# Kernel optimization log

Hardware: AMD Instinct MI355X
Metric: run time of the kernel (lower is better)

## Reference

```python
import jax, jax.numpy as jnp
import numpy as np

N = 8192
IN_F = 128
OUT_F = 128
ALPHA = 0.2  # LeakyReLU negative slope
NEG_INF = -9e15


def setup_inputs() -> dict:
    key = jax.random.key(0)
    k1, k2, k3, k4 = jax.random.split(key, 4)
    h = jax.random.normal(k1, (N, IN_F), dtype=jnp.float32)
    adj = jax.random.randint(k2, (N, N), 0, 2, dtype=jnp.int32)
    # nn.Linear(in, out, bias=False).weight is (out, in); store as (in, out) for h @ W
    W = jax.random.normal(k3, (IN_F, OUT_F), dtype=jnp.float32) * (1.0 / np.sqrt(IN_F))
    # a: (2*out_features, 1), xavier_uniform with gain=1.414
    limit = 1.414 * np.sqrt(6.0 / (2 * OUT_F + 1))
    a = jax.random.uniform(k4, (2 * OUT_F, 1), dtype=jnp.float32, minval=-limit, maxval=limit)
    return {"h": h, "adj": adj, "W": W, "a": a}


def reference(h, adj, W, a):
    Wh = h @ W  # (N, OUT_F)
    a1 = a[:OUT_F, 0]   # score contribution from source node i
    a2 = a[OUT_F:, 0]   # score contribution from target node j
    # e_ij = leakyrelu(Wh_i . a1 + Wh_j . a2) -- avoids the O(N^2 * 2F) concat
    s1 = Wh @ a1  # (N,)
    s2 = Wh @ a2  # (N,)
    e = jax.nn.leaky_relu(s1[:, None] + s2[None, :], negative_slope=ALPHA)  # (N, N)
    masked = jnp.where(adj > 0, e, NEG_INF)
    attention = jax.nn.softmax(masked, axis=1)  # (N, N)
    # dropout is a no-op in eval mode
    h_prime = attention @ Wh  # (N, OUT_F)
    return jax.nn.elu(h_prime)  # concat=True -> ELU
```

## Files before the change

### kernel.cpp

```cpp
#include <hip/hip_runtime.h>
#include <cstdint>
#include <cstddef>


#define NROW 8192
#define FDIM 128

typedef _Float16 f16;
typedef f16 f16x8 __attribute__((ext_vector_type(8)));
typedef float f32x4 __attribute__((ext_vector_type(4)));
typedef float f32x16 __attribute__((ext_vector_type(16)));

#define WS_BP  (2u*1024u*1024u)
#define WS_S12 (4u*1024u*1024u)
#define WS_RC  (WS_S12 + 64u*1024u)
#define WS_EF  (WS_RC + 128u*1024u)
#define WS_M2  (WS_EF + 64u*1024u)
#define WS_PWS (WS_M2 + 4u*1024u)

__global__ __launch_bounds__(256) void kA_wh_pack(const float* __restrict__ h,
                                                  const float* __restrict__ W,
                                                  const float* __restrict__ a,
                                                  const int* __restrict__ adj,
                                                  f16* __restrict__ Bp,
                                                  unsigned* __restrict__ bm,
                                                  float2* __restrict__ s12,
                                                  float* __restrict__ M2v) {
  __shared__ float smem[4736];
  const int bid = (int)blockIdx.x;
  const int t = (int)threadIdx.x;

  if (bid >= 256) {
    const int pb = bid - 256;
    const int w = t >> 6, l = t & 63;
    const int r = pb * 4 + w;
    const int rg = r >> 5, m = r & 31;
    const int* ap = adj + (size_t)r * NROW;
    unsigned* bp = bm + (size_t)rg * (256 * 32) + m;
    const int g = l >> 3;
    for (int jb = 0; jb < NROW; jb += 256) {
      int4 v = *(const int4*)(ap + jb + 4 * l);
      unsigned nib = (v.x > 0 ? 1u : 0u) | (v.y > 0 ? 2u : 0u) |
                     (v.z > 0 ? 4u : 0u) | (v.w > 0 ? 8u : 0u);
      unsigned word = nib << (4 * (l & 7));
      word |= (unsigned)__shfl_xor((int)word, 1, 64);
      word |= (unsigned)__shfl_xor((int)word, 2, 64);
      word |= (unsigned)__shfl_xor((int)word, 4, 64);
      if ((l & 7) == 0) bp[(size_t)((jb >> 5) + g) * 32] = word;
    }
    return;
  }

  const int rb = bid * 32;
  const f32x4* hv = (const f32x4*)(h + (size_t)rb * FDIM);
#pragma unroll
  for (int i = 0; i < 4; ++i) {
    int fidx = t + i * 256;
    f32x4 v = hv[fidx];
    int e0 = fidx * 4;
    int r = e0 >> 7, k = e0 & 127;
    smem[(k + 0) * 36 + r] = v[0];
    smem[(k + 1) * 36 + r] = v[1];
    smem[(k + 2) * 36 + r] = v[2];
    smem[(k + 3) * 36 + r] = v[3];
  }
  __syncthreads();
  const int f = t & 127, rh = t >> 7;
  f32x4 z = {0.f, 0.f, 0.f, 0.f};
  f32x4 acc0 = z, acc1 = z, acc2 = z, acc3 = z;
  for (int k = 0; k < 128; ++k) {
    float w = W[k * FDIM + f];
    const f32x4* hp = (const f32x4*)(smem + k * 36 + rh * 16);
    acc0 += hp[0] * w;
    acc1 += hp[1] * w;
    acc2 += hp[2] * w;
    acc3 += hp[3] * w;
  }
  union { f16 hx[16]; uint4 u[2]; } pk;
#pragma unroll
  for (int q = 0; q < 4; ++q) {
    pk.hx[0 + q]  = (f16)acc0[q];
    pk.hx[4 + q]  = (f16)acc1[q];
    pk.hx[8 + q]  = (f16)acc2[q];
    pk.hx[12 + q] = (f16)acc3[q];
  }
  f16* bdst = Bp + ((size_t)((bid * 2 + rh) * 4 + (f >> 5)) * 64 + (f & 31)) * 8;
  *(uint4*)bdst = pk.u[0];
  *(uint4*)(bdst + 256) = pk.u[1];

  __syncthreads();
#pragma unroll
  for (int q = 0; q < 4; ++q) {
    smem[(rh * 16 + 0  + q) * 132 + f] = acc0[q];
    smem[(rh * 16 + 4  + q) * 132 + f] = acc1[q];
    smem[(rh * 16 + 8  + q) * 132 + f] = acc2[q];
    smem[(rh * 16 + 12 + q) * 132 + f] = acc3[q];
  }
  __syncthreads();
  {
    const int row = t & 31, fc = t >> 5;
    const float* wrow = smem + row * 132 + fc * 16;
    float s1 = 0.f, s2 = 0.f;
#pragma unroll
    for (int ff = 0; ff < 16; ++ff) {
      float wv = wrow[ff];
      int fg = fc * 16 + ff;
      s1 = fmaf(wv, a[fg], s1);
      s2 = fmaf(wv, a[128 + fg], s2);
    }
    float* part = smem + 4224;
    __syncthreads();
    part[0 * 256 + fc * 32 + row] = s1;
    part[1 * 256 + fc * 32 + row] = s2;
    __syncthreads();
    if (t < 32) {
      float s1t = 0.f, s2t = 0.f;
#pragma unroll
      for (int c2 = 0; c2 < 8; ++c2) {
        s1t += part[c2 * 32 + t];
        s2t += part[256 + c2 * 32 + t];
      }
      s12[rb + t] = make_float2(s1t, s2t);
      float mx = s2t;
#pragma unroll
      for (int off = 16; off; off >>= 1) mx = fmaxf(mx, __shfl_xor(mx, off, 64));
      if (t == 0) M2v[bid] = mx;
    }
  }
}

__global__ __launch_bounds__(256) void k1c_prep(const float2* __restrict__ s12,
                                                const float* __restrict__ M2v,
                                                float4* __restrict__ RC,
                                                float2* __restrict__ EF) {
  __shared__ float red[4];
  const int t = (int)threadIdx.x;
  float v = M2v[t];
#pragma unroll
  for (int off = 32; off; off >>= 1) v = fmaxf(v, __shfl_xor(v, off, 64));
  if ((t & 63) == 0) red[t >> 6] = v;
  __syncthreads();
  float M2 = fmaxf(fmaxf(red[0], red[1]), fmaxf(red[2], red[3]));
  int j = (int)blockIdx.x * 256 + t;
  float2 s = s12[j];
  float c = s.x + M2;
  c = fmaxf(c, 0.2f * c);
  RC[j] = make_float4(__expf(-s.x), __expf(s.x - c), __expf(0.2f * s.x - c), 0.f);
  EF[j] = make_float2(__expf(s.y), __expf(0.2f * s.y));
}

__global__ __launch_bounds__(256) void k2_main(const unsigned* __restrict__ bm,
                                               const f16* __restrict__ Bp,
                                               const float4* __restrict__ RC,
                                               const float* __restrict__ EF,
                                               float* __restrict__ Pws,
                                               float* __restrict__ Dws,
                                               int jspan) {
  const int tid = (int)threadIdx.x;
  const int L = tid & 63, w = tid >> 6;
  const int wid = (int)blockIdx.x * 4 + w;
  const int rg = wid & 255;
  const int c = wid >> 8;
  const int rb = rg * 32;
  const int m = L & 31, kb = L >> 5;
  const int row = rb + m;
  const int j0 = c * jspan;
  const int niter = jspan >> 5;

  const float4 rc = RC[row];
  const float tau = rc.x, kap1 = rc.y, kap2 = rc.z;

  const unsigned* wbase = bm + ((size_t)rg * 256 + (size_t)(j0 >> 5)) * 32 + m;
  const f32x4* ep = (const f32x4*)(EF + 2 * (j0 + kb * 8));
  const f16* bp = Bp + (size_t)(j0 >> 4) * 2048 + L * 8;

  unsigned WD  = wbase[0];
  unsigned WDn = wbase[32];
  f32x4 E0 = ep[0], E1 = ep[1], E2 = ep[2], E3 = ep[3];
  f32x4 E4 = ep[8], E5 = ep[9], E6 = ep[10], E7 = ep[11];

  f32x16 zz = {0.f};
  f32x16 acc[4] = {zz, zz, zz, zz};
  float dloc = 0.f;

  for (int it = 0; it < niter; ++it) {
    const f16* bt = bp + (size_t)it * 4096;
    f16x8 B00 = *(const f16x8*)(bt);
    f16x8 B01 = *(const f16x8*)(bt + 512);
    f16x8 B02 = *(const f16x8*)(bt + 1024);
    f16x8 B03 = *(const f16x8*)(bt + 1536);
    f16x8 B10 = *(const f16x8*)(bt + 2048);
    f16x8 B11 = *(const f16x8*)(bt + 2560);
    f16x8 B12 = *(const f16x8*)(bt + 3072);
    f16x8 B13 = *(const f16x8*)(bt + 3584);

    const unsigned u0 = WD >> (kb * 8);
    const unsigned u1 = u0 >> 16;
    f16x8 af0, af1;
    {
      float p;
      p = (E0[0] > tau) ? E0[0] * kap1 : E0[1] * kap2; p = (u0 & 1u)   ? p : 0.f; dloc += p; af0[0] = (f16)p;
      p = (E0[2] > tau) ? E0[2] * kap1 : E0[3] * kap2; p = (u0 & 2u)   ? p : 0.f; dloc += p; af0[1] = (f16)p;
      p = (E1[0] > tau) ? E1[0] * kap1 : E1[1] * kap2; p = (u0 & 4u)   ? p : 0.f; dloc += p; af0[2] = (f16)p;
      p = (E1[2] > tau) ? E1[2] * kap1 : E1[3] * kap2; p = (u0 & 8u)   ? p : 0.f; dloc += p; af0[3] = (f16)p;
      p = (E2[0] > tau) ? E2[0] * kap1 : E2[1] * kap2; p = (u0 & 16u)  ? p : 0.f; dloc += p; af0[4] = (f16)p;
      p = (E2[2] > tau) ? E2[2] * kap1 : E2[3] * kap2; p = (u0 & 32u)  ? p : 0.f; dloc += p; af0[5] = (f16)p;
      p = (E3[0] > tau) ? E3[0] * kap1 : E3[1] * kap2; p = (u0 & 64u)  ? p : 0.f; dloc += p; af0[6] = (f16)p;
      p = (E3[2] > tau) ? E3[2] * kap1 : E3[3] * kap2; p = (u0 & 128u) ? p : 0.f; dloc += p; af0[7] = (f16)p;
      p = (E4[0] > tau) ? E4[0] * kap1 : E4[1] * kap2; p = (u1 & 1u)   ? p : 0.f; dloc += p; af1[0] = (f16)p;
      p = (E4[2] > tau) ? E4[2] * kap1 : E4[3] * kap2; p = (u1 & 2u)   ? p : 0.f; dloc += p; af1[1] = (f16)p;
      p = (E5[0] > tau) ? E5[0] * kap1 : E5[1] * kap2; p = (u1 & 4u)   ? p : 0.f; dloc += p; af1[2] = (f16)p;
      p = (E5[2] > tau) ? E5[2] * kap1 : E5[3] * kap2; p = (u1 & 8u)   ? p : 0.f; dloc += p; af1[3] = (f16)p;
      p = (E6[0] > tau) ? E6[0] * kap1 : E6[1] * kap2; p = (u1 & 16u)  ? p : 0.f; dloc += p; af1[4] = (f16)p;
      p = (E6[2] > tau) ? E6[2] * kap1 : E6[3] * kap2; p = (u1 & 32u)  ? p : 0.f; dloc += p; af1[5] = (f16)p;
      p = (E7[0] > tau) ? E7[0] * kap1 : E7[1] * kap2; p = (u1 & 64u)  ? p : 0.f; dloc += p; af1[6] = (f16)p;
      p = (E7[2] > tau) ? E7[2] * kap1 : E7[3] * kap2; p = (u1 & 128u) ? p : 0.f; dloc += p; af1[7] = (f16)p;
    }

    int nx = (it + 2 < niter) ? (it + 2) : (niter - 1);
    WD = WDn;
    WDn = wbase[(size_t)nx * 32];
    int adv = (it < niter - 1) ? 1 : 0;
    ep += adv * 16;
    E0 = ep[0]; E1 = ep[1]; E2 = ep[2]; E3 = ep[3];
    E4 = ep[8]; E5 = ep[9]; E6 = ep[10]; E7 = ep[11];

    __builtin_amdgcn_s_setprio(1);
    acc[0] = __builtin_amdgcn_mfma_f32_32x32x16_f16(af0, B00, acc[0], 0, 0, 0);
    acc[1] = __builtin_amdgcn_mfma_f32_32x32x16_f16(af0, B01, acc[1], 0, 0, 0);
    acc[2] = __builtin_amdgcn_mfma_f32_32x32x16_f16(af0, B02, acc[2], 0, 0, 0);
    acc[3] = __builtin_amdgcn_mfma_f32_32x32x16_f16(af0, B03, acc[3], 0, 0, 0);
    acc[0] = __builtin_amdgcn_mfma_f32_32x32x16_f16(af1, B10, acc[0], 0, 0, 0);
    acc[1] = __builtin_amdgcn_mfma_f32_32x32x16_f16(af1, B11, acc[1], 0, 0, 0);
    acc[2] = __builtin_amdgcn_mfma_f32_32x32x16_f16(af1, B12, acc[2], 0, 0, 0);
    acc[3] = __builtin_amdgcn_mfma_f32_32x32x16_f16(af1, B13, acc[3], 0, 0, 0);
    __builtin_amdgcn_s_setprio(0);
  }

  dloc += __shfl_xor(dloc, 32, 64);
  if (L < 32) Dws[(size_t)c * NROW + row] = dloc;

  float* P = Pws + ((size_t)c * NROW + rb) * FDIM + (L & 31);
#pragma unroll
  for (int nt = 0; nt < 4; ++nt) {
#pragma unroll
    for (int reg = 0; reg < 16; ++reg) {
      int rr = (reg & 3) + 8 * (reg >> 2) + 4 * kb;
      P[(size_t)rr * FDIM + nt * 32] = acc[nt][reg];
    }
  }
}

__global__ __launch_bounds__(256) void k3_comb(const float* __restrict__ Pws,
                                               const float* __restrict__ Dws,
                                               float* __restrict__ out, int S) {
  int g = (int)blockIdx.x * 256 + (int)threadIdx.x;
  int r = g >> 5, f4 = g & 31;
  f32x4 s = {0.f, 0.f, 0.f, 0.f};
  float den = 0.f;
  for (int c2 = 0; c2 < S; ++c2) {
    s += *(const f32x4*)(Pws + ((size_t)c2 * NROW + r) * FDIM + f4 * 4);
    den += Dws[(size_t)c2 * NROW + r];
  }
  float inv = 1.0f / den;
  f32x4 o;
#pragma unroll
  for (int e = 0; e < 4; ++e) {
    float x = s[e] * inv;
    o[e] = x > 0.f ? x : expm1f(x);
  }
  *(f32x4*)(out + (size_t)r * FDIM + f4 * 4) = o;
}

extern "C" void kernel_launch(void* const* d_in, const int* in_sizes, int n_in,
                              void* d_out, int out_size, void* d_ws, size_t ws_size,
                              hipStream_t stream) {
  const float* h = (const float*)d_in[0];
  const int* adj = (const int*)d_in[1];
  const float* W = (const float*)d_in[2];
  const float* a = (const float*)d_in[3];
  float* out = (float*)d_out;
  char* ws = (char*)d_ws;
  f16* Bp = (f16*)(ws + WS_BP);
  float2* s12 = (float2*)(ws + WS_S12);
  float4* RC = (float4*)(ws + WS_RC);
  float2* EF = (float2*)(ws + WS_EF);
  float* M2v = (float*)(ws + WS_M2);

  const size_t partial_bytes = (size_t)NROW * FDIM * 4;
  const size_t bm_bytes = (size_t)8 * 1024 * 1024;
  int S = (ws_size >= WS_PWS + 8 * partial_bytes + 8 * (size_t)NROW * 4 + bm_bytes) ? 8 : 2;
  float* Pws = (float*)(ws + WS_PWS);
  float* Dws = (float*)(ws + WS_PWS + (size_t)S * partial_bytes);
  unsigned* BM = (unsigned*)(ws + WS_PWS + (size_t)S * partial_bytes + (size_t)S * NROW * 4);
  int jspan = NROW / S;

  kA_wh_pack<<<dim3(2304), dim3(256), 0, stream>>>(h, W, a, adj, Bp, BM, s12, M2v);
  k1c_prep<<<dim3(32), dim3(256), 0, stream>>>(s12, M2v, RC, EF);
  k2_main<<<dim3(64 * S), dim3(256), 0, stream>>>(BM, Bp, RC, (const float*)EF, Pws, Dws, jspan);
  k3_comb<<<dim3(1024), dim3(256), 0, stream>>>(Pws, Dws, out, S);
}
```

Measured before the change: 431.0 us.

## Fuse adjacency bitmask packing into the main attention kernel

Removes the separate pass that packed the int32 adjacency matrix into a bitmask workspace. The main MFMA kernel now reads adj rows directly, one iteration ahead, and builds each row's 32-bit mask word in registers with cross-lane shuffles. This avoids writing and re-reading the bitmask and drops the extra packing blocks from the first kernel, so the adj stream overlaps with the matrix math. In exchange, the main kernel must stream the full 256 MB int32 matrix itself with limited occupancy and shallow prefetch, and it adds shuffle work per iteration. A redundant barrier in the Wh kernel is also dropped.

```diff
diff --git a/kernel.cpp b/kernel.cpp
--- a/kernel.cpp
+++ b/kernel.cpp
@@ -18,38 +18,15 @@
 #define WS_M2  (WS_EF + 64u*1024u)
 #define WS_PWS (WS_M2 + 4u*1024u)
 
-__global__ __launch_bounds__(256) void kA_wh_pack(const float* __restrict__ h,
-                                                  const float* __restrict__ W,
-                                                  const float* __restrict__ a,
-                                                  const int* __restrict__ adj,
-                                                  f16* __restrict__ Bp,
-                                                  unsigned* __restrict__ bm,
-                                                  float2* __restrict__ s12,
-                                                  float* __restrict__ M2v) {
+__global__ __launch_bounds__(256) void kA_wh(const float* __restrict__ h,
+                                             const float* __restrict__ W,
+                                             const float* __restrict__ a,
+                                             f16* __restrict__ Bp,
+                                             float2* __restrict__ s12,
+                                             float* __restrict__ M2v) {
   __shared__ float smem[4736];
   const int bid = (int)blockIdx.x;
   const int t = (int)threadIdx.x;
-
-  if (bid >= 256) {
-    const int pb = bid - 256;
-    const int w = t >> 6, l = t & 63;
-    const int r = pb * 4 + w;
-    const int rg = r >> 5, m = r & 31;
-    const int* ap = adj + (size_t)r * NROW;
-    unsigned* bp = bm + (size_t)rg * (256 * 32) + m;
-    const int g = l >> 3;
-    for (int jb = 0; jb < NROW; jb += 256) {
-      int4 v = *(const int4*)(ap + jb + 4 * l);
-      unsigned nib = (v.x > 0 ? 1u : 0u) | (v.y > 0 ? 2u : 0u) |
-                     (v.z > 0 ? 4u : 0u) | (v.w > 0 ? 8u : 0u);
-      unsigned word = nib << (4 * (l & 7));
-      word |= (unsigned)__shfl_xor((int)word, 1, 64);
-      word |= (unsigned)__shfl_xor((int)word, 2, 64);
-      word |= (unsigned)__shfl_xor((int)word, 4, 64);
-      if ((l & 7) == 0) bp[(size_t)((jb >> 5) + g) * 32] = word;
-    }
-    return;
-  }
 
   const int rb = bid * 32;
   const f32x4* hv = (const f32x4*)(h + (size_t)rb * FDIM);
@@ -109,7 +86,6 @@
       s2 = fmaf(wv, a[128 + fg], s2);
     }
     float* part = smem + 4224;
-    __syncthreads();
     part[0 * 256 + fc * 32 + row] = s1;
     part[1 * 256 + fc * 32 + row] = s2;
     __syncthreads();
@@ -149,7 +125,7 @@
   EF[j] = make_float2(__expf(s.y), __expf(0.2f * s.y));
 }
 
-__global__ __launch_bounds__(256) void k2_main(const unsigned* __restrict__ bm,
+__global__ __launch_bounds__(256) void k2_main(const int* __restrict__ adj,
                                                const f16* __restrict__ Bp,
                                                const float4* __restrict__ RC,
                                                const float* __restrict__ EF,
@@ -170,18 +146,23 @@
   const float4 rc = RC[row];
   const float tau = rc.x, kap1 = rc.y, kap2 = rc.z;
 
-  const unsigned* wbase = bm + ((size_t)rg * 256 + (size_t)(j0 >> 5)) * 32 + m;
+  const int* arow = adj + (size_t)(rb + (L >> 3)) * NROW + j0 + 4 * (L & 7);
   const f32x4* ep = (const f32x4*)(EF + 2 * (j0 + kb * 8));
   const f16* bp = Bp + (size_t)(j0 >> 4) * 2048 + L * 8;
 
-  unsigned WD  = wbase[0];
-  unsigned WDn = wbase[32];
+  int4 A0n = *(const int4*)(arow);
+  int4 A1n = *(const int4*)(arow + 8 * NROW);
+  int4 A2n = *(const int4*)(arow + 16 * NROW);
+  int4 A3n = *(const int4*)(arow + 24 * NROW);
   f32x4 E0 = ep[0], E1 = ep[1], E2 = ep[2], E3 = ep[3];
   f32x4 E4 = ep[8], E5 = ep[9], E6 = ep[10], E7 = ep[11];
 
   f32x16 zz = {0.f};
   f32x16 acc[4] = {zz, zz, zz, zz};
   float dloc = 0.f;
+
+  const int shmt = 4 * (L & 7);
+  const int srcl = 8 * (L & 7) + ((L >> 3) & 7);
 
   for (int it = 0; it < niter; ++it) {
     const f16* bt = bp + (size_t)it * 4096;
@@ -193,6 +174,38 @@
     f16x8 B11 = *(const f16x8*)(bt + 2560);
     f16x8 B12 = *(const f16x8*)(bt + 3072);
     f16x8 B13 = *(const f16x8*)(bt + 3584);
+
+    int4 A0 = A0n, A1 = A1n, A2 = A2n, A3 = A3n;
+    int nxo = ((it + 1 < niter) ? (it + 1) : it) * 32;
+    A0n = *(const int4*)(arow + nxo);
+    A1n = *(const int4*)(arow + 8 * NROW + nxo);
+    A2n = *(const int4*)(arow + 16 * NROW + nxo);
+    A3n = *(const int4*)(arow + 24 * NROW + nxo);
+
+    unsigned W0 = ((A0.x > 0 ? 1u : 0u) | (A0.y > 0 ? 2u : 0u) |
+                   (A0.z > 0 ? 4u : 0u) | (A0.w > 0 ? 8u : 0u)) << shmt;
+    unsigned W1 = ((A1.x > 0 ? 1u : 0u) | (A1.y > 0 ? 2u : 0u) |
+                   (A1.z > 0 ? 4u : 0u) | (A1.w > 0 ? 8u : 0u)) << shmt;
+    unsigned W2 = ((A2.x > 0 ? 1u : 0u) | (A2.y > 0 ? 2u : 0u) |
+                   (A2.z > 0 ? 4u : 0u) | (A2.w > 0 ? 8u : 0u)) << shmt;
+    unsigned W3 = ((A3.x > 0 ? 1u : 0u) | (A3.y > 0 ? 2u : 0u) |
+                   (A3.z > 0 ? 4u : 0u) | (A3.w > 0 ? 8u : 0u)) << shmt;
+    W0 |= (unsigned)__shfl_xor((int)W0, 1, 64);
+    W1 |= (unsigned)__shfl_xor((int)W1, 1, 64);
+    W2 |= (unsigned)__shfl_xor((int)W2, 1, 64);
+    W3 |= (unsigned)__shfl_xor((int)W3, 1, 64);
+    W0 |= (unsigned)__shfl_xor((int)W0, 2, 64);
+    W1 |= (unsigned)__shfl_xor((int)W1, 2, 64);
+    W2 |= (unsigned)__shfl_xor((int)W2, 2, 64);
+    W3 |= (unsigned)__shfl_xor((int)W3, 2, 64);
+    W0 |= (unsigned)__shfl_xor((int)W0, 4, 64);
+    W1 |= (unsigned)__shfl_xor((int)W1, 4, 64);
+    W2 |= (unsigned)__shfl_xor((int)W2, 4, 64);
+    W3 |= (unsigned)__shfl_xor((int)W3, 4, 64);
+    unsigned a01 = (L & 1) ? W1 : W0;
+    unsigned a23 = (L & 1) ? W3 : W2;
+    unsigned wsel = (L & 2) ? a23 : a01;
+    unsigned WD = (unsigned)__shfl((int)wsel, srcl, 64);
 
     const unsigned u0 = WD >> (kb * 8);
     const unsigned u1 = u0 >> 16;
@@ -217,9 +230,6 @@
       p = (E7[2] > tau) ? E7[2] * kap1 : E7[3] * kap2; p = (u1 & 128u) ? p : 0.f; dloc += p; af1[7] = (f16)p;
     }
 
-    int nx = (it + 2 < niter) ? (it + 2) : (niter - 1);
-    WD = WDn;
-    WDn = wbase[(size_t)nx * 32];
     int adv = (it < niter - 1) ? 1 : 0;
     ep += adv * 16;
     E0 = ep[0]; E1 = ep[1]; E2 = ep[2]; E3 = ep[3];
@@ -288,15 +298,13 @@
   float* M2v = (float*)(ws + WS_M2);
 
   const size_t partial_bytes = (size_t)NROW * FDIM * 4;
-  const size_t bm_bytes = (size_t)8 * 1024 * 1024;
-  int S = (ws_size >= WS_PWS + 8 * partial_bytes + 8 * (size_t)NROW * 4 + bm_bytes) ? 8 : 2;
+  int S = (ws_size >= WS_PWS + 8 * partial_bytes + 8 * (size_t)NROW * 4) ? 8 : 2;
   float* Pws = (float*)(ws + WS_PWS);
   float* Dws = (float*)(ws + WS_PWS + (size_t)S * partial_bytes);
-  unsigned* BM = (unsigned*)(ws + WS_PWS + (size_t)S * partial_bytes + (size_t)S * NROW * 4);
   int jspan = NROW / S;
 
-  kA_wh_pack<<<dim3(2304), dim3(256), 0, stream>>>(h, W, a, adj, Bp, BM, s12, M2v);
+  kA_wh<<<dim3(256), dim3(256), 0, stream>>>(h, W, a, Bp, s12, M2v);
   k1c_prep<<<dim3(32), dim3(256), 0, stream>>>(s12, M2v, RC, EF);
-  k2_main<<<dim3(64 * S), dim3(256), 0, stream>>>(BM, Bp, RC, (const float*)EF, Pws, Dws, jspan);
+  k2_main<<<dim3(64 * S), dim3(256), 0, stream>>>(adj, Bp, RC, (const float*)EF, Pws, Dws, jspan);
   k3_comb<<<dim3(1024), dim3(256), 0, stream>>>(Pws, Dws, out, S);
 }
```

After: 451.4 us. 4.7% more time.

## Fuse adjacency bitmask packing into main attention kernel with prefetch pipeline

Applied to the files above, without the earlier changes.

Removes the separate adjacency-to-bitmask pass from the first kernel. The main MFMA kernel now reads the int32 adjacency rows directly, packs them with wave ballots into per-row bitmasks, and prefetches the next 256-column superblock while computing the current one. This saves writing and re-reading an 8 MB bitmask and one pass over adj, at the cost of more registers and a more complex software pipeline. It also raises the column split to 16 when workspace allows, sets launch_bounds occupancy to 2, and drops a redundant barrier.

```diff
diff --git a/kernel.cpp b/kernel.cpp
--- a/kernel.cpp
+++ b/kernel.cpp
@@ -18,38 +18,15 @@
 #define WS_M2  (WS_EF + 64u*1024u)
 #define WS_PWS (WS_M2 + 4u*1024u)
 
-__global__ __launch_bounds__(256) void kA_wh_pack(const float* __restrict__ h,
-                                                  const float* __restrict__ W,
-                                                  const float* __restrict__ a,
-                                                  const int* __restrict__ adj,
-                                                  f16* __restrict__ Bp,
-                                                  unsigned* __restrict__ bm,
-                                                  float2* __restrict__ s12,
-                                                  float* __restrict__ M2v) {
+__global__ __launch_bounds__(256) void kA_wh(const float* __restrict__ h,
+                                             const float* __restrict__ W,
+                                             const float* __restrict__ a,
+                                             f16* __restrict__ Bp,
+                                             float2* __restrict__ s12,
+                                             float* __restrict__ M2v) {
   __shared__ float smem[4736];
   const int bid = (int)blockIdx.x;
   const int t = (int)threadIdx.x;
-
-  if (bid >= 256) {
-    const int pb = bid - 256;
-    const int w = t >> 6, l = t & 63;
-    const int r = pb * 4 + w;
-    const int rg = r >> 5, m = r & 31;
-    const int* ap = adj + (size_t)r * NROW;
-    unsigned* bp = bm + (size_t)rg * (256 * 32) + m;
-    const int g = l >> 3;
-    for (int jb = 0; jb < NROW; jb += 256) {
-      int4 v = *(const int4*)(ap + jb + 4 * l);
-      unsigned nib = (v.x > 0 ? 1u : 0u) | (v.y > 0 ? 2u : 0u) |
-                     (v.z > 0 ? 4u : 0u) | (v.w > 0 ? 8u : 0u);
-      unsigned word = nib << (4 * (l & 7));
-      word |= (unsigned)__shfl_xor((int)word, 1, 64);
-      word |= (unsigned)__shfl_xor((int)word, 2, 64);
-      word |= (unsigned)__shfl_xor((int)word, 4, 64);
-      if ((l & 7) == 0) bp[(size_t)((jb >> 5) + g) * 32] = word;
-    }
-    return;
-  }
 
   const int rb = bid * 32;
   const f32x4* hv = (const f32x4*)(h + (size_t)rb * FDIM);
@@ -109,7 +86,6 @@
       s2 = fmaf(wv, a[128 + fg], s2);
     }
     float* part = smem + 4224;
-    __syncthreads();
     part[0 * 256 + fc * 32 + row] = s1;
     part[1 * 256 + fc * 32 + row] = s2;
     __syncthreads();
@@ -149,13 +125,13 @@
   EF[j] = make_float2(__expf(s.y), __expf(0.2f * s.y));
 }
 
-__global__ __launch_bounds__(256) void k2_main(const unsigned* __restrict__ bm,
-                                               const f16* __restrict__ Bp,
-                                               const float4* __restrict__ RC,
-                                               const float* __restrict__ EF,
-                                               float* __restrict__ Pws,
-                                               float* __restrict__ Dws,
-                                               int jspan) {
+__global__ __launch_bounds__(256, 2) void k2_main(const int* __restrict__ adj,
+                                                  const f16* __restrict__ Bp,
+                                                  const float4* __restrict__ RC,
+                                                  const float* __restrict__ EF,
+                                                  float* __restrict__ Pws,
+                                                  float* __restrict__ Dws,
+                                                  int jspan) {
   const int tid = (int)threadIdx.x;
   const int L = tid & 63, w = tid >> 6;
   const int wid = (int)blockIdx.x * 4 + w;
@@ -165,17 +141,16 @@
   const int m = L & 31, kb = L >> 5;
   const int row = rb + m;
   const int j0 = c * jspan;
-  const int niter = jspan >> 5;
+  const int nsup = jspan >> 8;
 
   const float4 rc = RC[row];
   const float tau = rc.x, kap1 = rc.y, kap2 = rc.z;
-
-  const unsigned* wbase = bm + ((size_t)rg * 256 + (size_t)(j0 >> 5)) * 32 + m;
+  const unsigned kb2 = (unsigned)(kb * 2);
+
+  const int* abase = adj + (size_t)rb * NROW + j0 + 4 * L;
   const f32x4* ep = (const f32x4*)(EF + 2 * (j0 + kb * 8));
   const f16* bp = Bp + (size_t)(j0 >> 4) * 2048 + L * 8;
 
-  unsigned WD  = wbase[0];
-  unsigned WDn = wbase[32];
   f32x4 E0 = ep[0], E1 = ep[1], E2 = ep[2], E3 = ep[3];
   f32x4 E4 = ep[8], E5 = ep[9], E6 = ep[10], E7 = ep[11];
 
@@ -183,58 +158,148 @@
   f32x16 acc[4] = {zz, zz, zz, zz};
   float dloc = 0.f;
 
-  for (int it = 0; it < niter; ++it) {
-    const f16* bt = bp + (size_t)it * 4096;
-    f16x8 B00 = *(const f16x8*)(bt);
-    f16x8 B01 = *(const f16x8*)(bt + 512);
-    f16x8 B02 = *(const f16x8*)(bt + 1024);
-    f16x8 B03 = *(const f16x8*)(bt + 1536);
-    f16x8 B10 = *(const f16x8*)(bt + 2048);
-    f16x8 B11 = *(const f16x8*)(bt + 2560);
-    f16x8 B12 = *(const f16x8*)(bt + 3072);
-    f16x8 B13 = *(const f16x8*)(bt + 3584);
-
-    const unsigned u0 = WD >> (kb * 8);
-    const unsigned u1 = u0 >> 16;
-    f16x8 af0, af1;
+  unsigned Wl0 = 0, Wl1 = 0, Wl2 = 0, Wl3 = 0, Wh0 = 0, Wh1 = 0, Wh2 = 0, Wh3 = 0;
+  unsigned Nl0 = 0, Nl1 = 0, Nl2 = 0, Nl3 = 0, Nh0 = 0, Nh1 = 0, Nh2 = 0, Nh3 = 0;
+  int4 Ra0, Ra1, Ra2, Ra3;
+  int4 Rb0, Rb1, Rb2, Rb3;
+  int itile = 0;
+
+#define ISSUE4(QA, QB, QC, QD, k, scol) do {                         \
+    const int* ap_ = abase + (size_t)(4 * (k)) * NROW + (scol);      \
+    QA = *(const int4*)(ap_);                                        \
+    QB = *(const int4*)(ap_ + NROW);                                 \
+    QC = *(const int4*)(ap_ + 2 * NROW);                             \
+    QD = *(const int4*)(ap_ + 3 * NROW);                             \
+  } while (0)
+
+#define PACKROW(Q, r, DL0, DL1, DL2, DL3, DH0, DH1, DH2, DH3) do {   \
+    unsigned long long b0_ = __ballot((Q).x > 0);                    \
+    unsigned long long b1_ = __ballot((Q).y > 0);                    \
+    unsigned long long b2_ = __ballot((Q).z > 0);                    \
+    unsigned long long b3_ = __ballot((Q).w > 0);                    \
+    if (m == (r)) {                                                  \
+      DL0 = (unsigned)b0_; DH0 = (unsigned)(b0_ >> 32);              \
+      DL1 = (unsigned)b1_; DH1 = (unsigned)(b1_ >> 32);              \
+      DL2 = (unsigned)b2_; DH2 = (unsigned)(b2_ >> 32);              \
+      DL3 = (unsigned)b3_; DH3 = (unsigned)(b3_ >> 32);              \
+    }                                                                \
+  } while (0)
+
+#define PACK4(QA, QB, QC, QD, k, DL0, DL1, DL2, DL3, DH0, DH1, DH2, DH3) do { \
+    PACKROW(QA, 4 * (k) + 0, DL0, DL1, DL2, DL3, DH0, DH1, DH2, DH3);         \
+    PACKROW(QB, 4 * (k) + 1, DL0, DL1, DL2, DL3, DH0, DH1, DH2, DH3);         \
+    PACKROW(QC, 4 * (k) + 2, DL0, DL1, DL2, DL3, DH0, DH1, DH2, DH3);         \
+    PACKROW(QD, 4 * (k) + 3, DL0, DL1, DL2, DL3, DH0, DH1, DH2, DH3);         \
+  } while (0)
+
+#define TILE(tt, SL0, SL1, SL2, SL3, SH0, SH1, SH2, SH3) do {        \
+    const f16* bt = bp + (size_t)itile * 4096;                       \
+    f16x8 B00 = *(const f16x8*)(bt);                                 \
+    f16x8 B01 = *(const f16x8*)(bt + 512);                           \
+    f16x8 B02 = *(const f16x8*)(bt + 1024);                          \
+    f16x8 B03 = *(const f16x8*)(bt + 1536);                          \
+    f16x8 B10 = *(const f16x8*)(bt + 2048);                          \
+    f16x8 B11 = *(const f16x8*)(bt + 2560);                          \
+    f16x8 B12 = *(const f16x8*)(bt + 3072);                          \
+    f16x8 B13 = *(const f16x8*)(bt + 3584);                          \
+    unsigned sh_ = kb2 + 8u * ((tt) & 3);                            \
+    unsigned vb0 = (((tt) < 4) ? SL0 : SH0) >> sh_;                  \
+    unsigned vb1 = (((tt) < 4) ? SL1 : SH1) >> sh_;                  \
+    unsigned vb2 = (((tt) < 4) ? SL2 : SH2) >> sh_;                  \
+    unsigned vb3 = (((tt) < 4) ? SL3 : SH3) >> sh_;                  \
+    unsigned vc0 = vb0 >> 4, vc1 = vb1 >> 4, vc2 = vb2 >> 4, vc3 = vb3 >> 4; \
+    f16x8 af0, af1;                                                  \
+    { float p;                                                       \
+      p = (E0[0] > tau) ? E0[0] * kap1 : E0[1] * kap2; p = (vb0 & 1u) ? p : 0.f; dloc += p; af0[0] = (f16)p; \
+      p = (E0[2] > tau) ? E0[2] * kap1 : E0[3] * kap2; p = (vb1 & 1u) ? p : 0.f; dloc += p; af0[1] = (f16)p; \
+      p = (E1[0] > tau) ? E1[0] * kap1 : E1[1] * kap2; p = (vb2 & 1u) ? p : 0.f; dloc += p; af0[2] = (f16)p; \
+      p = (E1[2] > tau) ? E1[2] * kap1 : E1[3] * kap2; p = (vb3 & 1u) ? p : 0.f; dloc += p; af0[3] = (f16)p; \
+      p = (E2[0] > tau) ? E2[0] * kap1 : E2[1] * kap2; p = (vb0 & 2u) ? p : 0.f; dloc += p; af0[4] = (f16)p; \
+      p = (E2[2] > tau) ? E2[2] * kap1 : E2[3] * kap2; p = (vb1 & 2u) ? p : 0.f; dloc += p; af0[5] = (f16)p; \
+      p = (E3[0] > tau) ? E3[0] * kap1 : E3[1] * kap2; p = (vb2 & 2u) ? p : 0.f; dloc += p; af0[6] = (f16)p; \
+      p = (E3[2] > tau) ? E3[2] * kap1 : E3[3] * kap2; p = (vb3 & 2u) ? p : 0.f; dloc += p; af0[7] = (f16)p; \
+      p = (E4[0] > tau) ? E4[0] * kap1 : E4[1] * kap2; p = (vc0 & 1u) ? p : 0.f; dloc += p; af1[0] = (f16)p; \
+      p = (E4[2] > tau) ? E4[2] * kap1 : E4[3] * kap2; p = (vc1 & 1u) ? p : 0.f; dloc += p; af1[1] = (f16)p; \
+      p = (E5[0] > tau) ? E5[0] * kap1 : E5[1] * kap2; p = (vc2 & 1u) ? p : 0.f; dloc += p; af1[2] = (f16)p; \
+      p = (E5[2] > tau) ? E5[2] * kap1 : E5[3] * kap2; p = (vc3 & 1u) ? p : 0.f; dloc += p; af1[3] = (f16)p; \
+      p = (E6[0] > tau) ? E6[0] * kap1 : E6[1] * kap2; p = (vc0 & 2u) ? p : 0.f; dloc += p; af1[4] = (f16)p; \
+      p = (E6[2] > tau) ? E6[2] * kap1 : E6[3] * kap2; p = (vc1 & 2u) ? p : 0.f; dloc += p; af1[5] = (f16)p; \
+      p = (E7[0] > tau) ? E7[0] * kap1 : E7[1] * kap2; p = (vc2 & 2u) ? p : 0.f; dloc += p; af1[6] = (f16)p; \
+      p = (E7[2] > tau) ? E7[2] * kap1 : E7[3] * kap2; p = (vc3 & 2u) ? p : 0.f; dloc += p; af1[7] = (f16)p; \
+    }                                                                \
+    ep += 16;   \
+    E0 = ep[0]; E1 = ep[1]; E2 = ep[2]; E3 = ep[3];                  \
+    E4 = ep[8]; E5 = ep[9]; E6 = ep[10]; E7 = ep[11];                \
+    __builtin_amdgcn_s_setprio(1);                                   \
+    acc[0] = __builtin_amdgcn_mfma_f32_32x32x16_f16(af0, B00, acc[0], 0, 0, 0); \
+    acc[1] = __builtin_amdgcn_mfma_f32_32x32x16_f16(af0, B01, acc[1], 0, 0, 0); \
+    acc[2] = __builtin_amdgcn_mfma_f32_32x32x16_f16(af0, B02, acc[2], 0, 0, 0); \
+    acc[3] = __builtin_amdgcn_mfma_f32_32x32x16_f16(af0, B03, acc[3], 0, 0, 0); \
+    acc[0] = __builtin_amdgcn_mfma_f32_32x32x16_f16(af1, B10, acc[0], 0, 0, 0); \
+    acc[1] = __builtin_amdgcn_mfma_f32_32x32x16_f16(af1, B11, acc[1], 0, 0, 0); \
+    acc[2] = __builtin_amdgcn_mfma_f32_32x32x16_f16(af1, B12, acc[2], 0, 0, 0); \
+    acc[3] = __builtin_amdgcn_mfma_f32_32x32x16_f16(af1, B13, acc[3], 0, 0, 0); \
+    __builtin_amdgcn_s_setprio(0);                                   \
+    ++itile;                                                         \
+  } while (0)
+
+#define SUPER(SL0, SL1, SL2, SL3, SH0, SH1, SH2, SH3,                \
+              NL0, NL1, NL2, NL3, NH0, NH1, NH2, NH3, hasn, scoln) do {       \
+    TILE(0, SL0, SL1, SL2, SL3, SH0, SH1, SH2, SH3);                          \
+    if (hasn) ISSUE4(Ra0, Ra1, Ra2, Ra3, 0, scoln);                           \
+    TILE(1, SL0, SL1, SL2, SL3, SH0, SH1, SH2, SH3);                          \
+    if (hasn) ISSUE4(Rb0, Rb1, Rb2, Rb3, 1, scoln);                           \
+    if (hasn) PACK4(Ra0, Ra1, Ra2, Ra3, 0, NL0, NL1, NL2, NL3, NH0, NH1, NH2, NH3); \
+    TILE(2, SL0, SL1, SL2, SL3, SH0, SH1, SH2, SH3);                          \
+    if (hasn) ISSUE4(Ra0, Ra1, Ra2, Ra3, 2, scoln);                           \
+    if (hasn) PACK4(Rb0, Rb1, Rb2, Rb3, 1, NL0, NL1, NL2, NL3, NH0, NH1, NH2, NH3); \
+    TILE(3, SL0, SL1, SL2, SL3, SH0, SH1, SH2, SH3);                          \
+    if (hasn) ISSUE4(Rb0, Rb1, Rb2, Rb3, 3, scoln);                           \
+    if (hasn) PACK4(Ra0, Ra1, Ra2, Ra3, 2, NL0, NL1, NL2, NL3, NH0, NH1, NH2, NH3); \
+    TILE(4, SL0, SL1, SL2, SL3, SH0, SH1, SH2, SH3);                          \
+    if (hasn) ISSUE4(Ra0, Ra1, Ra2, Ra3, 4, scoln);                           \
+    if (hasn) PACK4(Rb0, Rb1, Rb2, Rb3, 3, NL0, NL1, NL2, NL3, NH0, NH1, NH2, NH3); \
+    TILE(5, SL0, SL1, SL2, SL3, SH0, SH1, SH2, SH3);                          \
+    if (hasn) ISSUE4(Rb0, Rb1, Rb2, Rb3, 5, scoln);                           \
+    if (hasn) PACK4(Ra0, Ra1, Ra2, Ra3, 4, NL0, NL1, NL2, NL3, NH0, NH1, NH2, NH3); \
+    TILE(6, SL0, SL1, SL2, SL3, SH0, SH1, SH2, SH3);                          \
+    if (hasn) ISSUE4(Ra0, Ra1, Ra2, Ra3, 6, scoln);                           \
+    if (hasn) PACK4(Rb0, Rb1, Rb2, Rb3, 5, NL0, NL1, NL2, NL3, NH0, NH1, NH2, NH3); \
+    TILE(7, SL0, SL1, SL2, SL3, SH0, SH1, SH2, SH3);                          \
+    if (hasn) ISSUE4(Rb0, Rb1, Rb2, Rb3, 7, scoln);                           \
+    if (hasn) PACK4(Ra0, Ra1, Ra2, Ra3, 6, NL0, NL1, NL2, NL3, NH0, NH1, NH2, NH3); \
+    if (hasn) PACK4(Rb0, Rb1, Rb2, Rb3, 7, NL0, NL1, NL2, NL3, NH0, NH1, NH2, NH3); \
+  } while (0)
+
+  ISSUE4(Ra0, Ra1, Ra2, Ra3, 0, 0);
+  ISSUE4(Rb0, Rb1, Rb2, Rb3, 1, 0);
+  PACK4(Ra0, Ra1, Ra2, Ra3, 0, Wl0, Wl1, Wl2, Wl3, Wh0, Wh1, Wh2, Wh3);
+  ISSUE4(Ra0, Ra1, Ra2, Ra3, 2, 0);
+  PACK4(Rb0, Rb1, Rb2, Rb3, 1, Wl0, Wl1, Wl2, Wl3, Wh0, Wh1, Wh2, Wh3);
+  ISSUE4(Rb0, Rb1, Rb2, Rb3, 3, 0);
+  PACK4(Ra0, Ra1, Ra2, Ra3, 2, Wl0, Wl1, Wl2, Wl3, Wh0, Wh1, Wh2, Wh3);
+  ISSUE4(Ra0, Ra1, Ra2, Ra3, 4, 0);
+  PACK4(Rb0, Rb1, Rb2, Rb3, 3, Wl0, Wl1, Wl2, Wl3, Wh0, Wh1, Wh2, Wh3);
+  ISSUE4(Rb0, Rb1, Rb2, Rb3, 5, 0);
+  PACK4(Ra0, Ra1, Ra2, Ra3, 4, Wl0, Wl1, Wl2, Wl3, Wh0, Wh1, Wh2, Wh3);
+  ISSUE4(Ra0, Ra1, Ra2, Ra3, 6, 0);
+  PACK4(Rb0, Rb1, Rb2, Rb3, 5, Wl0, Wl1, Wl2, Wl3, Wh0, Wh1, Wh2, Wh3);
+  ISSUE4(Rb0, Rb1, Rb2, Rb3, 7, 0);
+  PACK4(Ra0, Ra1, Ra2, Ra3, 6, Wl0, Wl1, Wl2, Wl3, Wh0, Wh1, Wh2, Wh3);
+  PACK4(Rb0, Rb1, Rb2, Rb3, 7, Wl0, Wl1, Wl2, Wl3, Wh0, Wh1, Wh2, Wh3);
+
+  for (int ss = 0; ss < nsup; ss += 2) {
     {
-      float p;
-      p = (E0[0] > tau) ? E0[0] * kap1 : E0[1] * kap2; p = (u0 & 1u)   ? p : 0.f; dloc += p; af0[0] = (f16)p;
-      p = (E0[2] > tau) ? E0[2] * kap1 : E0[3] * kap2; p = (u0 & 2u)   ? p : 0.f; dloc += p; af0[1] = (f16)p;
-      p = (E1[0] > tau) ? E1[0] * kap1 : E1[1] * kap2; p = (u0 & 4u)   ? p : 0.f; dloc += p; af0[2] = (f16)p;
-      p = (E1[2] > tau) ? E1[2] * kap1 : E1[3] * kap2; p = (u0 & 8u)   ? p : 0.f; dloc += p; af0[3] = (f16)p;
-      p = (E2[0] > tau) ? E2[0] * kap1 : E2[1] * kap2; p = (u0 & 16u)  ? p : 0.f; dloc += p; af0[4] = (f16)p;
-      p = (E2[2] > tau) ? E2[2] * kap1 : E2[3] * kap2; p = (u0 & 32u)  ? p : 0.f; dloc += p; af0[5] = (f16)p;
-      p = (E3[0] > tau) ? E3[0] * kap1 : E3[1] * kap2; p = (u0 & 64u)  ? p : 0.f; dloc += p; af0[6] = (f16)p;
-      p = (E3[2] > tau) ? E3[2] * kap1 : E3[3] * kap2; p = (u0 & 128u) ? p : 0.f; dloc += p; af0[7] = (f16)p;
-      p = (E4[0] > tau) ? E4[0] * kap1 : E4[1] * kap2; p = (u1 & 1u)   ? p : 0.f; dloc += p; af1[0] = (f16)p;
-      p = (E4[2] > tau) ? E4[2] * kap1 : E4[3] * kap2; p = (u1 & 2u)   ? p : 0.f; dloc += p; af1[1] = (f16)p;
-      p = (E5[0] > tau) ? E5[0] * kap1 : E5[1] * kap2; p = (u1 & 4u)   ? p : 0.f; dloc += p; af1[2] = (f16)p;
-      p = (E5[2] > tau) ? E5[2] * kap1 : E5[3] * kap2; p = (u1 & 8u)   ? p : 0.f; dloc += p; af1[3] = (f16)p;
-      p = (E6[0] > tau) ? E6[0] * kap1 : E6[1] * kap2; p = (u1 & 16u)  ? p : 0.f; dloc += p; af1[4] = (f16)p;
-      p = (E6[2] > tau) ? E6[2] * kap1 : E6[3] * kap2; p = (u1 & 32u)  ? p : 0.f; dloc += p; af1[5] = (f16)p;
-      p = (E7[0] > tau) ? E7[0] * kap1 : E7[1] * kap2; p = (u1 & 64u)  ? p : 0.f; dloc += p; af1[6] = (f16)p;
-      p = (E7[2] > tau) ? E7[2] * kap1 : E7[3] * kap2; p = (u1 & 128u) ? p : 0.f; dloc += p; af1[7] = (f16)p;
-    }
-
-    int nx = (it + 2 < niter) ? (it + 2) : (niter - 1);
-    WD = WDn;
-    WDn = wbase[(size_t)nx * 32];
-    int adv = (it < niter - 1) ? 1 : 0;
-    ep += adv * 16;
-    E0 = ep[0]; E1 = ep[1]; E2 = ep[2]; E3 = ep[3];
-    E4 = ep[8]; E5 = ep[9]; E6 = ep[10]; E7 = ep[11];
-
-    __builtin_amdgcn_s_setprio(1);
-    acc[0] = __builtin_amdgcn_mfma_f32_32x32x16_f16(af0, B00, acc[0], 0, 0, 0);
-    acc[1] = __builtin_amdgcn_mfma_f32_32x32x16_f16(af0, B01, acc[1], 0, 0, 0);
-    acc[2] = __builtin_amdgcn_mfma_f32_32x32x16_f16(af0, B02, acc[2], 0, 0, 0);
-    acc[3] = __builtin_amdgcn_mfma_f32_32x32x16_f16(af0, B03, acc[3], 0, 0, 0);
-    acc[0] = __builtin_amdgcn_mfma_f32_32x32x16_f16(af1, B10, acc[0], 0, 0, 0);
-    acc[1] = __builtin_amdgcn_mfma_f32_32x32x16_f16(af1, B11, acc[1], 0, 0, 0);
-    acc[2] = __builtin_amdgcn_mfma_f32_32x32x16_f16(af1, B12, acc[2], 0, 0, 0);
-    acc[3] = __builtin_amdgcn_mfma_f32_32x32x16_f16(af1, B13, acc[3], 0, 0, 0);
-    __builtin_amdgcn_s_setprio(0);
+      int scoln = (ss + 1) * 256;
+      SUPER(Wl0, Wl1, Wl2, Wl3, Wh0, Wh1, Wh2, Wh3,
+            Nl0, Nl1, Nl2, Nl3, Nh0, Nh1, Nh2, Nh3, true, scoln);
+    }
+    {
+      const bool hasn = (ss + 2) < nsup;
+      int scoln = hasn ? (ss + 2) * 256 : 0;
+      SUPER(Nl0, Nl1, Nl2, Nl3, Nh0, Nh1, Nh2, Nh3,
+            Wl0, Wl1, Wl2, Wl3, Wh0, Wh1, Wh2, Wh3, hasn, scoln);
+    }
   }
 
   dloc += __shfl_xor(dloc, 32, 64);
@@ -288,15 +353,15 @@
   float* M2v = (float*)(ws + WS_M2);
 
   const size_t partial_bytes = (size_t)NROW * FDIM * 4;
-  const size_t bm_bytes = (size_t)8 * 1024 * 1024;
-  int S = (ws_size >= WS_PWS + 8 * partial_bytes + 8 * (size_t)NROW * 4 + bm_bytes) ? 8 : 2;
+  int S = 2;
+  if (ws_size >= WS_PWS + 16 * partial_bytes + 16 * (size_t)NROW * 4) S = 16;
+  else if (ws_size >= WS_PWS + 8 * partial_bytes + 8 * (size_t)NROW * 4) S = 8;
   float* Pws = (float*)(ws + WS_PWS);
   float* Dws = (float*)(ws + WS_PWS + (size_t)S * partial_bytes);
-  unsigned* BM = (unsigned*)(ws + WS_PWS + (size_t)S * partial_bytes + (size_t)S * NROW * 4);
   int jspan = NROW / S;
 
-  kA_wh_pack<<<dim3(2304), dim3(256), 0, stream>>>(h, W, a, adj, Bp, BM, s12, M2v);
+  kA_wh<<<dim3(256), dim3(256), 0, stream>>>(h, W, a, Bp, s12, M2v);
   k1c_prep<<<dim3(32), dim3(256), 0, stream>>>(s12, M2v, RC, EF);
-  k2_main<<<dim3(64 * S), dim3(256), 0, stream>>>(BM, Bp, RC, (const float*)EF, Pws, Dws, jspan);
+  k2_main<<<dim3(64 * S), dim3(256), 0, stream>>>(adj, Bp, RC, (const float*)EF, Pws, Dws, jspan);
   k3_comb<<<dim3(1024), dim3(256), 0, stream>>>(Pws, Dws, out, S);
 }
```

Result: slower. 695.9 us (+61.5%).
